# Performance work log

Hardware: AMD Instinct MI355X
Metric: run time of the kernel (lower is better)

Reference implementation:

```python
import jax, jax.numpy as jnp
import numpy as np

B, S, H, L = 8, 4096, 768, 256   # batch, seq_len, hidden_size, num_lines (= line_ids.max()+1)
ATT_HID = 1024                    # attention MLP hidden dim from nn.Linear(hidden,1024)


def setup_inputs() -> dict:
    key = jax.random.key(0)
    k0, k1, k2, k3 = jax.random.split(key, 4)
    token_hidden = jax.random.normal(k0, (B, S, H), dtype=jnp.float32)
    line_ids = jax.random.randint(k1, (B, S), 0, L)  # all valid; -1 would mark invalid
    W1 = jax.random.normal(k2, (H, ATT_HID), dtype=jnp.float32) * 0.02
    b1 = jnp.zeros((ATT_HID,), jnp.float32)
    W2 = jax.random.normal(k3, (ATT_HID, 1), dtype=jnp.float32) * 0.02
    b2 = jnp.zeros((1,), jnp.float32)
    return {"token_hidden": token_hidden, "line_ids": line_ids,
            "W1": W1, "b1": b1, "W2": W2, "b2": b2}


def reference(token_hidden, line_ids, W1, b1, W2, b2):
    b, s, h = token_hidden.shape
    num_lines = L
    n_seg = b * num_lines + 1  # last segment is a dump slot for invalid (-1) tokens

    # attention scores: Linear -> tanh -> Linear, squeeze(-1)  [b, s]
    scores = (jnp.tanh(token_hidden @ W1 + b1) @ W2 + b2)[..., 0]

    valid = (line_ids >= 0).reshape(-1)                                   # [b*s]
    seg = jnp.where(line_ids >= 0,
                    jnp.arange(b)[:, None] * num_lines + line_ids,
                    b * num_lines).reshape(-1)                            # [b*s]
    s_flat = jnp.where(valid, scores.reshape(-1), -jnp.inf)

    # segment-wise stable softmax
    m = jax.ops.segment_max(s_flat, seg, num_segments=n_seg)
    m = jnp.where(jnp.isfinite(m), m, 0.0)  # empty segments -> safe 0
    e = jnp.where(valid, jnp.exp(scores.reshape(-1) - m[seg]), 0.0)
    denom = jax.ops.segment_sum(e, seg, num_segments=n_seg)
    w = e / jnp.maximum(denom[seg], 1e-20)                                # [b*s]

    # weighted sum of tokens per (batch, line) segment
    feats = jax.ops.segment_sum(token_hidden.reshape(-1, h) * w[:, None],
                                seg, num_segments=n_seg)
    line_features = feats[: b * num_lines].reshape(b, num_lines, h)

    counts = jax.ops.segment_sum(valid.astype(jnp.float32), seg, num_segments=n_seg)
    line_mask = counts[: b * num_lines].reshape(b, num_lines) > 0
    return line_features, line_mask
```

## Files before the change

kernel.cpp:

```cpp
#include <hip/hip_runtime.h>
#include <hip/hip_bf16.h>
#include <string.h>

#define M_TOK 32768
#define H_DIM 768
#define AH    1024
#define NSEG  2048
#define LCAP  192
#define CONV_BLOCKS 12288
#define NKT   12

typedef __attribute__((ext_vector_type(8))) __bf16 bf16x8;
typedef __attribute__((ext_vector_type(4))) float f32x4;

__device__ __forceinline__ float tanh_fast(float x) {
  float e = __expf(2.0f * x);
  return 1.0f - 2.0f * __builtin_amdgcn_rcpf(e + 1.0f);
}

__device__ __forceinline__ float bf2f(unsigned short u) {
  unsigned int v = (unsigned int)u << 16;
  float f;
  memcpy(&f, &v, 4);
  return f;
}

__global__ __launch_bounds__(256) void prep_kernel(
    const float* __restrict__ W1, __hip_bfloat16* __restrict__ W1t,
    const float4* __restrict__ X4, uint4* __restrict__ Xb4) {
  __shared__ float tile[32][33];
  if (blockIdx.x < 768) {
    int nt = blockIdx.x & 31, ktile = blockIdx.x >> 5;
    int n0 = nt * 32, k0 = ktile * 32;
    int tx = threadIdx.x & 31, ty = threadIdx.x >> 5;
    for (int r = ty; r < 32; r += 8)
      tile[r][tx] = W1[(size_t)(k0 + r) * AH + n0 + tx];
    __syncthreads();
    for (int r = ty; r < 32; r += 8)
      W1t[(size_t)(n0 + r) * H_DIM + k0 + tx] = __float2bfloat16(tile[tx][r]);
  } else {
    int i = (blockIdx.x - 768) * 256 + threadIdx.x;
    float4 v0 = X4[i * 2];
    float4 v1 = X4[i * 2 + 1];
    __hip_bfloat16 h[8] = {
        __float2bfloat16(v0.x), __float2bfloat16(v0.y),
        __float2bfloat16(v0.z), __float2bfloat16(v0.w),
        __float2bfloat16(v1.x), __float2bfloat16(v1.y),
        __float2bfloat16(v1.z), __float2bfloat16(v1.w)};
    uint4 p;
    memcpy(&p, h, 16);
    Xb4[i] = p;
  }
}

#define WAITV(N) asm volatile("s_waitcnt vmcnt(" #N ")" ::: "memory")
#define WAITL0   asm volatile("s_waitcnt lgkmcnt(0)" ::: "memory")

__global__ __launch_bounds__(512, 2) void attn_score_kernel(
    const __hip_bfloat16* __restrict__ Xbg,
    const __hip_bfloat16* __restrict__ W1tg, const float* __restrict__ b1g,
    const float* __restrict__ W2g, float* __restrict__ scores2) {
  __shared__ __align__(16) __bf16 As[2][256 * 64];
  __shared__ __align__(16) __bf16 Bs[2][256 * 64];

  const int tid = threadIdx.x;
  const int bid = blockIdx.x;
  const int xcd = bid & 7;
  const int sq  = bid >> 3;
  const int m0  = (xcd * 16 + (sq >> 2)) * 256;
  const int ntl = sq & 3;
  const int n0  = ntl * 256;
  const int lane = tid & 63;
  const int wave = tid >> 6;
  const int wm   = wave >> 2;
  const int wx   = wave & 3;
  const int ml   = lane & 15;
  const int lh   = lane >> 4;

  const __bf16* Xb = (const __bf16*)Xbg;
  const __bf16* W  = (const __bf16*)W1tg;

  const int lr   = tid >> 3;
  const int scol = ((tid & 7) ^ (lr & 7)) << 3;

  int aRow[4], bRow[4];
#pragma unroll
  for (int q = 0; q < 4; ++q) {
    aRow[q] = m0 + ((q & 1) << 7) + ((q >> 1) << 6) + lr;
    int lrow = (q << 6) + lr;
    bRow[q] = n0 + (((lrow >> 5) & 3) << 6) + ((lrow >> 7) << 5) + (lrow & 31);
  }

  f32x4 acc[8][4];
#pragma unroll
  for (int i = 0; i < 8; ++i)
#pragma unroll
    for (int j = 0; j < 4; ++j) acc[i][j] = (f32x4)0.f;

#define STAGE_A(q, buf, kt)                                                    \
  __builtin_amdgcn_global_load_lds(                                            \
      (const __attribute__((address_space(1))) void*)(Xb +                     \
          (size_t)aRow[q] * H_DIM + (kt) + scol),                              \
      (__attribute__((address_space(3))) void*)&As[buf][(q) * 4096 + tid * 8], \
      16, 0, 0)
#define STAGE_B(q, buf, kt)                                                    \
  __builtin_amdgcn_global_load_lds(                                            \
      (const __attribute__((address_space(1))) void*)(W +                      \
          (size_t)bRow[q] * H_DIM + (kt) + scol),                              \
      (__attribute__((address_space(3))) void*)&Bs[buf][(q) * 4096 + tid * 8], \
      16, 0, 0)

  STAGE_A(0, 0, 0); STAGE_A(1, 0, 0);
  STAGE_B(0, 0, 0); STAGE_B(1, 0, 0);
  STAGE_A(2, 0, 0); STAGE_A(3, 0, 0);
  STAGE_B(2, 0, 0); STAGE_B(3, 0, 0);

#define PHASE_BODY(Q, P, SS)                                                   \
  {                                                                            \
    __builtin_amdgcn_s_barrier();                                              \
    __builtin_amdgcn_sched_barrier(0);                                         \
    const int mh = (Q) & 1, nh = (Q) >> 1;                                     \
    bf16x8 af[4][2], bfr[2][2];                                                \
    _Pragma("unroll") for (int lf = 0; lf < 4; ++lf) {                         \
      int ra = (mh << 7) + (wm << 6) + (lf << 4) + ml;                         \
      _Pragma("unroll") for (int kk = 0; kk < 2; ++kk) {                       \
        int ph = ((kk << 2) + lh) ^ (ml & 7);                                  \
        af[lf][kk] = *(const bf16x8*)&As[P][(ra << 6) + (ph << 3)];            \
      }                                                                        \
    }                                                                          \
    _Pragma("unroll") for (int jj = 0; jj < 2; ++jj) {                         \
      int rb = (nh << 7) + (wx << 5) + (jj << 4) + ml;                         \
      _Pragma("unroll") for (int kk = 0; kk < 2; ++kk) {                       \
        int ph = ((kk << 2) + lh) ^ (ml & 7);                                  \
        bfr[jj][kk] = *(const bf16x8*)&Bs[P][(rb << 6) + (ph << 3)];           \
      }                                                                        \
    }                                                                          \
    SS;                                                                        \
    WAITL0;                                                                    \
    __builtin_amdgcn_sched_barrier(0);                                         \
    __builtin_amdgcn_s_setprio(1);                                             \
    _Pragma("unroll") for (int lf = 0; lf < 4; ++lf)                           \
      _Pragma("unroll") for (int jj = 0; jj < 2; ++jj)                         \
        _Pragma("unroll") for (int kk = 0; kk < 2; ++kk)                       \
          acc[mh * 4 + lf][nh * 2 + jj] =                                      \
              __builtin_amdgcn_mfma_f32_16x16x32_bf16(                         \
                  af[lf][kk], bfr[jj][kk], acc[mh * 4 + lf][nh * 2 + jj],      \
                  0, 0, 0);                                                    \
    __builtin_amdgcn_s_setprio(0);                                             \
  }

  int p = 0;
  for (int t = 0; t < NKT - 1; ++t) {
    const int ktn = (t + 1) << 6;
    WAITV(4);
    PHASE_BODY(0, p, { STAGE_A(0, p ^ 1, ktn); STAGE_A(1, p ^ 1, ktn); });
    WAITV(4);
    PHASE_BODY(1, p, { STAGE_B(0, p ^ 1, ktn); STAGE_B(1, p ^ 1, ktn); });
    WAITV(4);
    PHASE_BODY(2, p, { STAGE_A(2, p ^ 1, ktn); STAGE_A(3, p ^ 1, ktn); });
    PHASE_BODY(3, p, { STAGE_B(2, p ^ 1, ktn); STAGE_B(3, p ^ 1, ktn); });
    p ^= 1;
  }
  WAITV(4);
  PHASE_BODY(0, p, ((void)0));
  WAITV(2);
  PHASE_BODY(1, p, ((void)0));
  WAITV(0);
  PHASE_BODY(2, p, ((void)0));
  PHASE_BODY(3, p, ((void)0));

  float b1v[4], w2v[4];
#pragma unroll
  for (int nf = 0; nf < 4; ++nf) {
    int n = n0 + wx * 64 + nf * 16 + ml;
    b1v[nf] = b1g[n];
    w2v[nf] = W2g[n];
  }
  float* red = (float*)&As[0][0];
#pragma unroll
  for (int mf = 0; mf < 8; ++mf) {
#pragma unroll
    for (int pp = 0; pp < 4; ++pp) {
      float tsum = 0.f;
#pragma unroll
      for (int nf = 0; nf < 4; ++nf)
        tsum += tanh_fast(acc[mf][nf][pp] + b1v[nf]) * w2v[nf];
      tsum += __shfl_xor(tsum, 1);
      tsum += __shfl_xor(tsum, 2);
      tsum += __shfl_xor(tsum, 4);
      tsum += __shfl_xor(tsum, 8);
      if (ml == 0)
        red[wx * 256 + wm * 128 + mf * 16 + lh * 4 + pp] = tsum;
    }
  }
  __syncthreads();
  if (tid < 256) {
    float v = (red[tid] + red[256 + tid]) + (red[512 + tid] + red[768 + tid]);
    scores2[(size_t)(m0 + tid) * 4 + ntl] = v;
  }
}

__global__ __launch_bounds__(256) void aggregate_kernel(
    const ushort* __restrict__ Xb, const float* __restrict__ scores2,
    const int* __restrict__ line_ids, float4* __restrict__ out4,
    float* __restrict__ out_mask) {
  __shared__ int   slist[LCAP];
  __shared__ float sw[LCAP];
  __shared__ int   wvc[4];
  __shared__ float wred[4];
  const int seg = blockIdx.x;
  const int b = seg >> 8, lid = seg & 255;
  const int tid = threadIdx.x, lane = tid & 63, wave = tid >> 6;
  const int base = b * 4096;

  int ids[16];
#pragma unroll
  for (int c = 0; c < 16; ++c) ids[c] = line_ids[base + c * 256 + tid];

  int total = 0;
#pragma unroll
  for (int c = 0; c < 16; ++c) {
    bool match = (ids[c] == lid);
    unsigned long long mask = __ballot(match);
    if (lane == 0) wvc[wave] = __popcll(mask);
    __syncthreads();
    int off = total;
    for (int w = 0; w < wave; ++w) off += wvc[w];
    if (match) {
      int pos = off + __popcll(mask & ((1ull << lane) - 1ull));
      if (pos < LCAP) slist[pos] = base + c * 256 + tid;
    }
    total += wvc[0] + wvc[1] + wvc[2] + wvc[3];
    __syncthreads();
  }
  int cnt = total > LCAP ? LCAP : total;
  if (tid == 0) out_mask[seg] = cnt > 0 ? 1.f : 0.f;
  if (cnt == 0) {
    if (tid < H_DIM / 4)
      out4[(size_t)seg * (H_DIM / 4) + tid] = make_float4(0.f, 0.f, 0.f, 0.f);
    return;
  }
  float lmax = -3.4e38f;
  if (tid < cnt) {
    const float4 a = *(const float4*)(scores2 + (size_t)slist[tid] * 4);
    float sc = (a.x + a.y) + (a.z + a.w);
    sw[tid] = sc;
    lmax = sc;
  }
#pragma unroll
  for (int d = 1; d < 64; d <<= 1) lmax = fmaxf(lmax, __shfl_xor(lmax, d));
  if (lane == 0) wred[wave] = lmax;
  __syncthreads();
  float m = fmaxf(fmaxf(wred[0], wred[1]), fmaxf(wred[2], wred[3]));
  float lsum = 0.f;
  if (tid < cnt) {
    float e = __expf(sw[tid] - m);
    sw[tid] = e;
    lsum = e;
  }
#pragma unroll
  for (int d = 1; d < 64; d <<= 1) lsum += __shfl_xor(lsum, d);
  __syncthreads();
  if (lane == 0) wred[wave] = lsum;
  __syncthreads();
  float denom = wred[0] + wred[1] + wred[2] + wred[3];
  float inv = __builtin_amdgcn_rcpf(fmaxf(denom, 1e-20f));
  if (tid < cnt) sw[tid] *= inv;
  __syncthreads();
  if (tid < H_DIM / 4) {
    const ushort4* xb = (const ushort4*)Xb + tid;
    float4 acc = make_float4(0.f, 0.f, 0.f, 0.f);
    int t = 0;
    for (; t + 4 <= cnt; t += 4) {
      ushort4 u0 = xb[(size_t)slist[t]     * (H_DIM / 4)];
      ushort4 u1 = xb[(size_t)slist[t + 1] * (H_DIM / 4)];
      ushort4 u2 = xb[(size_t)slist[t + 2] * (H_DIM / 4)];
      ushort4 u3 = xb[(size_t)slist[t + 3] * (H_DIM / 4)];
      float w0 = sw[t], w1 = sw[t + 1], w2 = sw[t + 2], w3 = sw[t + 3];
      acc.x += w0 * bf2f(u0.x) + w1 * bf2f(u1.x) + w2 * bf2f(u2.x) + w3 * bf2f(u3.x);
      acc.y += w0 * bf2f(u0.y) + w1 * bf2f(u1.y) + w2 * bf2f(u2.y) + w3 * bf2f(u3.y);
      acc.z += w0 * bf2f(u0.z) + w1 * bf2f(u1.z) + w2 * bf2f(u2.z) + w3 * bf2f(u3.z);
      acc.w += w0 * bf2f(u0.w) + w1 * bf2f(u1.w) + w2 * bf2f(u2.w) + w3 * bf2f(u3.w);
    }
    for (; t < cnt; ++t) {
      ushort4 u = xb[(size_t)slist[t] * (H_DIM / 4)];
      float w = sw[t];
      acc.x += w * bf2f(u.x); acc.y += w * bf2f(u.y);
      acc.z += w * bf2f(u.z); acc.w += w * bf2f(u.w);
    }
    out4[(size_t)seg * (H_DIM / 4) + tid] = acc;
  }
}

extern "C" void kernel_launch(void* const* d_in, const int* in_sizes, int n_in,
                              void* d_out, int out_size, void* d_ws, size_t ws_size,
                              hipStream_t stream) {
  const float* X        = (const float*)d_in[0];
  const int*   line_ids = (const int*)d_in[1];
  const float* W1       = (const float*)d_in[2];
  const float* b1       = (const float*)d_in[3];
  const float* W2       = (const float*)d_in[4];

  char* p = (char*)d_ws;
  __hip_bfloat16* Xb      = (__hip_bfloat16*)p;  p += (size_t)M_TOK * H_DIM * 2;
  __hip_bfloat16* W1t     = (__hip_bfloat16*)p;  p += 1572864;
  float*          scores2 = (float*)p;           p += (size_t)M_TOK * 4 * 4;

  float* out_feats = (float*)d_out;
  float* out_mask  = out_feats + (size_t)NSEG * H_DIM;

  prep_kernel<<<768 + CONV_BLOCKS, 256, 0, stream>>>(
      W1, W1t, (const float4*)X, (uint4*)Xb);
  attn_score_kernel<<<512, 512, 0, stream>>>(Xb, W1t, b1, W2, scores2);
  aggregate_kernel<<<NSEG, 256, 0, stream>>>((const ushort*)Xb, scores2,
                                             line_ids, (float4*)out_feats,
                                             out_mask);
}
```

Before: 233.0 us.

## Process two N-tiles per block with a continuous pipelined K loop

Each score-GEMM block now covers 512 output columns instead of 256 by running the K loop twice in a single pipeline that flows from the first N half into the second, so the grid is halved to 256 blocks. The main loop is reorganised so fragment reads are reused across quadrants (A or B fragments kept between MFMA groups) and the LDS reads are issued before the barriers. An epilogue runs mid-loop for the first half. The aim is to cut the pipeline prologue and drain overhead per block and the number of LDS fragment reads. The cost is fewer blocks, which may leave CUs underused (256 blocks at 2 per CU), plus extra barriers.

New measurement: 235.7 us. Within noise of the previous version (+1.2%).

```diff
diff --git a/kernel.cpp b/kernel.cpp
--- a/kernel.cpp
+++ b/kernel.cpp
@@ -67,9 +67,8 @@
   const int bid = blockIdx.x;
   const int xcd = bid & 7;
   const int sq  = bid >> 3;
-  const int m0  = (xcd * 16 + (sq >> 2)) * 256;
-  const int ntl = sq & 3;
-  const int n0  = ntl * 256;
+  const int m0  = (xcd * 16 + (sq >> 1)) * 256;
+  const int np0 = (sq & 1) * 512;
   const int lane = tid & 63;
   const int wave = tid >> 6;
   const int wm   = wave >> 2;
@@ -88,7 +87,7 @@
   for (int q = 0; q < 4; ++q) {
     aRow[q] = m0 + ((q & 1) << 7) + ((q >> 1) << 6) + lr;
     int lrow = (q << 6) + lr;
-    bRow[q] = n0 + (((lrow >> 5) & 3) << 6) + ((lrow >> 7) << 5) + (lrow & 31);
+    bRow[q] = np0 + (((lrow >> 5) & 3) << 6) + ((lrow >> 7) << 5) + (lrow & 31);
   }
 
   f32x4 acc[8][4];
@@ -96,6 +95,19 @@
   for (int i = 0; i < 8; ++i)
 #pragma unroll
     for (int j = 0; j < 4; ++j) acc[i][j] = (f32x4)0.f;
+
+  bf16x8 af[4][2], bfr[2][2];
+
+  float b1v[2][4], w2v[2][4];
+#pragma unroll
+  for (int sd = 0; sd < 2; ++sd)
+#pragma unroll
+    for (int nf = 0; nf < 4; ++nf) {
+      int n = np0 + sd * 256 + wx * 64 + nf * 16 + ml;
+      b1v[sd][nf] = b1g[n];
+      w2v[sd][nf] = W2g[n];
+    }
+  WAITV(0);
 
 #define STAGE_A(q, buf, kt)                                                    \
   __builtin_amdgcn_global_load_lds(                                            \
@@ -103,101 +115,153 @@
           (size_t)aRow[q] * H_DIM + (kt) + scol),                              \
       (__attribute__((address_space(3))) void*)&As[buf][(q) * 4096 + tid * 8], \
       16, 0, 0)
-#define STAGE_B(q, buf, kt)                                                    \
+#define STAGE_B(q, buf, kt, nsh)                                               \
   __builtin_amdgcn_global_load_lds(                                            \
       (const __attribute__((address_space(1))) void*)(W +                      \
-          (size_t)bRow[q] * H_DIM + (kt) + scol),                              \
+          (size_t)(bRow[q] + (nsh)) * H_DIM + (kt) + scol),                    \
       (__attribute__((address_space(3))) void*)&Bs[buf][(q) * 4096 + tid * 8], \
       16, 0, 0)
 
-  STAGE_A(0, 0, 0); STAGE_A(1, 0, 0);
-  STAGE_B(0, 0, 0); STAGE_B(1, 0, 0);
-  STAGE_A(2, 0, 0); STAGE_A(3, 0, 0);
-  STAGE_B(2, 0, 0); STAGE_B(3, 0, 0);
-
-#define PHASE_BODY(Q, P, SS)                                                   \
+#define DSRA(MH, P)                                                            \
+  _Pragma("unroll") for (int lf = 0; lf < 4; ++lf) {                           \
+    int ra = ((MH) << 7) + (wm << 6) + (lf << 4) + ml;                         \
+    _Pragma("unroll") for (int kk = 0; kk < 2; ++kk) {                         \
+      int ph = ((kk << 2) + lh) ^ (ml & 7);                                    \
+      af[lf][kk] = *(const bf16x8*)&As[P][(ra << 6) + (ph << 3)];              \
+    }                                                                          \
+  }
+#define DSRB(NH, P)                                                            \
+  _Pragma("unroll") for (int jj = 0; jj < 2; ++jj) {                           \
+    int rb = ((NH) << 7) + (wx << 5) + (jj << 4) + ml;                         \
+    _Pragma("unroll") for (int kk = 0; kk < 2; ++kk) {                         \
+      int ph = ((kk << 2) + lh) ^ (ml & 7);                                    \
+      bfr[jj][kk] = *(const bf16x8*)&Bs[P][(rb << 6) + (ph << 3)];             \
+    }                                                                          \
+  }
+#define MFMAQ(MH, NH)                                                          \
+  __builtin_amdgcn_s_setprio(1);                                               \
+  _Pragma("unroll") for (int kk = 0; kk < 2; ++kk)                             \
+    _Pragma("unroll") for (int lf = 0; lf < 4; ++lf)                           \
+      _Pragma("unroll") for (int jj = 0; jj < 2; ++jj)                         \
+        acc[(MH) * 4 + lf][(NH) * 2 + jj] =                                    \
+            __builtin_amdgcn_mfma_f32_16x16x32_bf16(                           \
+                af[lf][kk], bfr[jj][kk], acc[(MH) * 4 + lf][(NH) * 2 + jj],    \
+                0, 0, 0);                                                      \
+  __builtin_amdgcn_s_setprio(0);
+
+#define BARRIER __builtin_amdgcn_s_barrier()
+#define SCHED0  __builtin_amdgcn_sched_barrier(0)
+
+#define EPILOGUE(side)                                                         \
   {                                                                            \
-    __builtin_amdgcn_s_barrier();                                              \
-    __builtin_amdgcn_sched_barrier(0);                                         \
-    const int mh = (Q) & 1, nh = (Q) >> 1;                                     \
-    bf16x8 af[4][2], bfr[2][2];                                                \
-    _Pragma("unroll") for (int lf = 0; lf < 4; ++lf) {                         \
-      int ra = (mh << 7) + (wm << 6) + (lf << 4) + ml;                         \
-      _Pragma("unroll") for (int kk = 0; kk < 2; ++kk) {                       \
-        int ph = ((kk << 2) + lh) ^ (ml & 7);                                  \
-        af[lf][kk] = *(const bf16x8*)&As[P][(ra << 6) + (ph << 3)];            \
+    __syncthreads();                                                           \
+    float* red = (float*)&As[1][0];                                            \
+    _Pragma("unroll") for (int mf = 0; mf < 8; ++mf) {                         \
+      _Pragma("unroll") for (int pp = 0; pp < 4; ++pp) {                       \
+        float tsum = 0.f;                                                      \
+        _Pragma("unroll") for (int nf = 0; nf < 4; ++nf)                       \
+          tsum += tanh_fast(acc[mf][nf][pp] + b1v[side][nf]) * w2v[side][nf];  \
+        tsum += __shfl_xor(tsum, 1);                                           \
+        tsum += __shfl_xor(tsum, 2);                                           \
+        tsum += __shfl_xor(tsum, 4);                                           \
+        tsum += __shfl_xor(tsum, 8);                                           \
+        if (ml == 0)                                                           \
+          red[wx * 256 + wm * 128 + mf * 16 + lh * 4 + pp] = tsum;             \
       }                                                                        \
     }                                                                          \
-    _Pragma("unroll") for (int jj = 0; jj < 2; ++jj) {                         \
-      int rb = (nh << 7) + (wx << 5) + (jj << 4) + ml;                         \
-      _Pragma("unroll") for (int kk = 0; kk < 2; ++kk) {                       \
-        int ph = ((kk << 2) + lh) ^ (ml & 7);                                  \
-        bfr[jj][kk] = *(const bf16x8*)&Bs[P][(rb << 6) + (ph << 3)];           \
-      }                                                                        \
+    __syncthreads();                                                           \
+    if (tid < 256) {                                                           \
+      float v =                                                                \
+          (red[tid] + red[256 + tid]) + (red[512 + tid] + red[768 + tid]);     \
+      scores2[(size_t)(m0 + tid) * 4 + ((sq & 1) * 2 + (side))] = v;           \
     }                                                                          \
-    SS;                                                                        \
-    WAITL0;                                                                    \
-    __builtin_amdgcn_sched_barrier(0);                                         \
-    __builtin_amdgcn_s_setprio(1);                                             \
-    _Pragma("unroll") for (int lf = 0; lf < 4; ++lf)                           \
-      _Pragma("unroll") for (int jj = 0; jj < 2; ++jj)                         \
-        _Pragma("unroll") for (int kk = 0; kk < 2; ++kk)                       \
-          acc[mh * 4 + lf][nh * 2 + jj] =                                      \
-              __builtin_amdgcn_mfma_f32_16x16x32_bf16(                         \
-                  af[lf][kk], bfr[jj][kk], acc[mh * 4 + lf][nh * 2 + jj],      \
-                  0, 0, 0);                                                    \
-    __builtin_amdgcn_s_setprio(0);                                             \
-  }
-
-  int p = 0;
-  for (int t = 0; t < NKT - 1; ++t) {
-    const int ktn = (t + 1) << 6;
+  }
+
+  STAGE_A(0, 0, 0); STAGE_A(1, 0, 0);
+  STAGE_B(0, 0, 0, 0); STAGE_B(1, 0, 0, 0);
+  STAGE_A(2, 0, 0); STAGE_A(3, 0, 0);
+  STAGE_B(2, 0, 0, 0); STAGE_B(3, 0, 0, 0);
+  WAITV(4);
+  BARRIER;
+
+  int P = 0;
+  for (int tt = 0; tt < 2 * NKT - 1; ++tt) {
+    const int u   = tt + 1;
+    const int ktu = ((u >= NKT) ? (u - NKT) : u) << 6;
+    const int nsh = (u >= NKT) ? 256 : 0;
+
+    DSRA(0, P); DSRB(0, P);
+    STAGE_A(0, P ^ 1, ktu); STAGE_A(1, P ^ 1, ktu);
+    asm volatile("s_waitcnt lgkmcnt(8)" ::: "memory");
+    BARRIER;
+    WAITL0; SCHED0;
+    MFMAQ(0, 0);
     WAITV(4);
-    PHASE_BODY(0, p, { STAGE_A(0, p ^ 1, ktn); STAGE_A(1, p ^ 1, ktn); });
+    BARRIER;
+
+    DSRA(1, P);
+    STAGE_B(0, P ^ 1, ktu, nsh); STAGE_B(1, P ^ 1, ktu, nsh);
+    BARRIER;
+    WAITL0; SCHED0;
+    MFMAQ(1, 0);
     WAITV(4);
-    PHASE_BODY(1, p, { STAGE_B(0, p ^ 1, ktn); STAGE_B(1, p ^ 1, ktn); });
+    BARRIER;
+
+    DSRB(1, P);
+    STAGE_A(2, P ^ 1, ktu); STAGE_A(3, P ^ 1, ktu);
+    BARRIER;
+    WAITL0; SCHED0;
+    MFMAQ(1, 1);
+    BARRIER;
+
+    DSRA(0, P);
+    STAGE_B(2, P ^ 1, ktu, nsh); STAGE_B(3, P ^ 1, ktu, nsh);
+    BARRIER;
+    WAITL0; SCHED0;
+    MFMAQ(0, 1);
     WAITV(4);
-    PHASE_BODY(2, p, { STAGE_A(2, p ^ 1, ktn); STAGE_A(3, p ^ 1, ktn); });
-    PHASE_BODY(3, p, { STAGE_B(2, p ^ 1, ktn); STAGE_B(3, p ^ 1, ktn); });
-    p ^= 1;
-  }
-  WAITV(4);
-  PHASE_BODY(0, p, ((void)0));
+    BARRIER;
+
+    P ^= 1;
+
+    if (tt == NKT - 1) {
+      EPILOGUE(0);
+#pragma unroll
+      for (int i = 0; i < 8; ++i)
+#pragma unroll
+        for (int j = 0; j < 4; ++j) acc[i][j] = (f32x4)0.f;
+      WAITV(0);
+      __syncthreads();
+    }
+  }
+
+  DSRA(0, 1); DSRB(0, 1);
+  asm volatile("s_waitcnt lgkmcnt(8)" ::: "memory");
+  BARRIER;
+  WAITL0; SCHED0;
+  MFMAQ(0, 0);
   WAITV(2);
-  PHASE_BODY(1, p, ((void)0));
+  BARRIER;
+
+  DSRA(1, 1);
+  BARRIER;
+  WAITL0; SCHED0;
+  MFMAQ(1, 0);
   WAITV(0);
-  PHASE_BODY(2, p, ((void)0));
-  PHASE_BODY(3, p, ((void)0));
-
-  float b1v[4], w2v[4];
-#pragma unroll
-  for (int nf = 0; nf < 4; ++nf) {
-    int n = n0 + wx * 64 + nf * 16 + ml;
-    b1v[nf] = b1g[n];
-    w2v[nf] = W2g[n];
-  }
-  float* red = (float*)&As[0][0];
-#pragma unroll
-  for (int mf = 0; mf < 8; ++mf) {
-#pragma unroll
-    for (int pp = 0; pp < 4; ++pp) {
-      float tsum = 0.f;
-#pragma unroll
-      for (int nf = 0; nf < 4; ++nf)
-        tsum += tanh_fast(acc[mf][nf][pp] + b1v[nf]) * w2v[nf];
-      tsum += __shfl_xor(tsum, 1);
-      tsum += __shfl_xor(tsum, 2);
-      tsum += __shfl_xor(tsum, 4);
-      tsum += __shfl_xor(tsum, 8);
-      if (ml == 0)
-        red[wx * 256 + wm * 128 + mf * 16 + lh * 4 + pp] = tsum;
-    }
-  }
-  __syncthreads();
-  if (tid < 256) {
-    float v = (red[tid] + red[256 + tid]) + (red[512 + tid] + red[768 + tid]);
-    scores2[(size_t)(m0 + tid) * 4 + ntl] = v;
-  }
+  BARRIER;
+
+  DSRB(1, 1);
+  BARRIER;
+  WAITL0; SCHED0;
+  MFMAQ(1, 1);
+  BARRIER;
+
+  DSRA(0, 1);
+  BARRIER;
+  WAITL0; SCHED0;
+  MFMAQ(0, 1);
+
+  EPILOGUE(1);
 }
 
 __global__ __launch_bounds__(256) void aggregate_kernel(
@@ -311,7 +375,7 @@
 
   prep_kernel<<<768 + CONV_BLOCKS, 256, 0, stream>>>(
       W1, W1t, (const float4*)X, (uint4*)Xb);
-  attn_score_kernel<<<512, 512, 0, stream>>>(Xb, W1t, b1, W2, scores2);
+  attn_score_kernel<<<256, 512, 0, stream>>>(Xb, W1t, b1, W2, scores2);
   aggregate_kernel<<<NSEG, 256, 0, stream>>>((const ushort*)Xb, scores2,
                                              line_ids, (float4*)out_feats,
                                              out_mask);
```

## Switch score GEMM to 32x32 MFMA with persistent two-pass N tiles per block

Applied to the files above, without the earlier changes.

The attention-score GEMM now uses 32x32x16 bf16 MFMA instead of 16x16x32. Each block covers 512 output columns in two sequential 256-column passes, running the tanh/W2 epilogue between them, so the grid halves to 256 blocks. The four-phase pipeline becomes a single double-buffered loop over 24 k-steps with precomputed pointers and LDS offsets. This aims to cut LDS fragment traffic and launch/tail overhead. In exchange only 256 blocks are launched, which lowers occupancy, and the single WAITV(0) per step may expose load latency.

New measurement: 253.2 us. 1.09x slower.

```diff
diff --git a/kernel.cpp b/kernel.cpp
--- a/kernel.cpp
+++ b/kernel.cpp
@@ -12,6 +12,7 @@
 
 typedef __attribute__((ext_vector_type(8))) __bf16 bf16x8;
 typedef __attribute__((ext_vector_type(4))) float f32x4;
+typedef __attribute__((ext_vector_type(16))) float f32x16;
 
 __device__ __forceinline__ float tanh_fast(float x) {
   float e = __expf(2.0f * x);
@@ -54,7 +55,6 @@
 }
 
 #define WAITV(N) asm volatile("s_waitcnt vmcnt(" #N ")" ::: "memory")
-#define WAITL0   asm volatile("s_waitcnt lgkmcnt(0)" ::: "memory")
 
 __global__ __launch_bounds__(512, 2) void attn_score_kernel(
     const __hip_bfloat16* __restrict__ Xbg,
@@ -67,15 +67,15 @@
   const int bid = blockIdx.x;
   const int xcd = bid & 7;
   const int sq  = bid >> 3;
-  const int m0  = (xcd * 16 + (sq >> 2)) * 256;
-  const int ntl = sq & 3;
-  const int n0  = ntl * 256;
+  const int m0  = (xcd * 16 + (sq >> 1)) * 256;
+  const int np0 = (sq & 1) * 512;
   const int lane = tid & 63;
   const int wave = tid >> 6;
   const int wm   = wave >> 2;
   const int wx   = wave & 3;
-  const int ml   = lane & 15;
-  const int lh   = lane >> 4;
+  const int l31  = lane & 31;
+  const int lk   = lane >> 5;
+  const int l7   = lane & 7;
 
   const __bf16* Xb = (const __bf16*)Xbg;
   const __bf16* W  = (const __bf16*)W1tg;
@@ -83,121 +83,128 @@
   const int lr   = tid >> 3;
   const int scol = ((tid & 7) ^ (lr & 7)) << 3;
 
-  int aRow[4], bRow[4];
+  const __bf16* aP[4];
+  const __bf16* bP[4];
 #pragma unroll
   for (int q = 0; q < 4; ++q) {
-    aRow[q] = m0 + ((q & 1) << 7) + ((q >> 1) << 6) + lr;
-    int lrow = (q << 6) + lr;
-    bRow[q] = n0 + (((lrow >> 5) & 3) << 6) + ((lrow >> 7) << 5) + (lrow & 31);
-  }
-
-  f32x4 acc[8][4];
-#pragma unroll
-  for (int i = 0; i < 8; ++i)
-#pragma unroll
-    for (int j = 0; j < 4; ++j) acc[i][j] = (f32x4)0.f;
-
-#define STAGE_A(q, buf, kt)                                                    \
+    aP[q] = Xb + (size_t)(m0 + (q << 6) + lr) * H_DIM + scol;
+    bP[q] = W + (size_t)(np0 + (q << 6) + lr) * H_DIM + scol;
+  }
+
+  int raBase[4], rbBase[2], physg[4];
+#pragma unroll
+  for (int p = 0; p < 4; ++p) raBase[p] = (wm * 128 + p * 32 + l31) << 6;
+#pragma unroll
+  for (int q = 0; q < 2; ++q) rbBase[q] = (wx * 64 + q * 32 + l31) << 6;
+#pragma unroll
+  for (int ks = 0; ks < 4; ++ks) physg[ks] = (((ks << 1) + lk) ^ l7) << 3;
+
+  f32x16 acc[4][2];
+#pragma unroll
+  for (int p = 0; p < 4; ++p)
+#pragma unroll
+    for (int q = 0; q < 2; ++q) acc[p][q] = (f32x16)0.f;
+
+  float b1v[2][2], w2v[2][2];
+#pragma unroll
+  for (int sd = 0; sd < 2; ++sd)
+#pragma unroll
+    for (int q = 0; q < 2; ++q) {
+      int n = np0 + sd * 256 + wx * 64 + q * 32 + l31;
+      b1v[sd][q] = b1g[n];
+      w2v[sd][q] = W2g[n];
+    }
+  WAITV(0);
+
+#define STAGE_A(q, buf, off)                                                   \
   __builtin_amdgcn_global_load_lds(                                            \
-      (const __attribute__((address_space(1))) void*)(Xb +                     \
-          (size_t)aRow[q] * H_DIM + (kt) + scol),                              \
+      (const __attribute__((address_space(1))) void*)(aP[q] + (off)),          \
       (__attribute__((address_space(3))) void*)&As[buf][(q) * 4096 + tid * 8], \
       16, 0, 0)
-#define STAGE_B(q, buf, kt)                                                    \
+#define STAGE_B(q, buf, off)                                                   \
   __builtin_amdgcn_global_load_lds(                                            \
-      (const __attribute__((address_space(1))) void*)(W +                      \
-          (size_t)bRow[q] * H_DIM + (kt) + scol),                              \
+      (const __attribute__((address_space(1))) void*)(bP[q] + (off)),          \
       (__attribute__((address_space(3))) void*)&Bs[buf][(q) * 4096 + tid * 8], \
       16, 0, 0)
 
-  STAGE_A(0, 0, 0); STAGE_A(1, 0, 0);
-  STAGE_B(0, 0, 0); STAGE_B(1, 0, 0);
-  STAGE_A(2, 0, 0); STAGE_A(3, 0, 0);
-  STAGE_B(2, 0, 0); STAGE_B(3, 0, 0);
-
-#define PHASE_BODY(Q, P, SS)                                                   \
+#define EPILOGUE(side)                                                         \
   {                                                                            \
-    __builtin_amdgcn_s_barrier();                                              \
-    __builtin_amdgcn_sched_barrier(0);                                         \
-    const int mh = (Q) & 1, nh = (Q) >> 1;                                     \
-    bf16x8 af[4][2], bfr[2][2];                                                \
-    _Pragma("unroll") for (int lf = 0; lf < 4; ++lf) {                         \
-      int ra = (mh << 7) + (wm << 6) + (lf << 4) + ml;                         \
-      _Pragma("unroll") for (int kk = 0; kk < 2; ++kk) {                       \
-        int ph = ((kk << 2) + lh) ^ (ml & 7);                                  \
-        af[lf][kk] = *(const bf16x8*)&As[P][(ra << 6) + (ph << 3)];            \
+    __syncthreads();                                                           \
+    float* red = (float*)&As[1][0];                                            \
+    _Pragma("unroll") for (int p = 0; p < 4; ++p) {                            \
+      _Pragma("unroll") for (int rg = 0; rg < 16; ++rg) {                      \
+        float v = tanh_fast(acc[p][0][rg] + b1v[side][0]) * w2v[side][0] +     \
+                  tanh_fast(acc[p][1][rg] + b1v[side][1]) * w2v[side][1];      \
+        v += __shfl_xor(v, 1);                                                 \
+        v += __shfl_xor(v, 2);                                                 \
+        v += __shfl_xor(v, 4);                                                 \
+        v += __shfl_xor(v, 8);                                                 \
+        v += __shfl_xor(v, 16);                                                \
+        if (l31 == 0) {                                                        \
+          int row = wm * 128 + p * 32 + (rg & 3) + ((rg >> 2) << 3) + (lk << 2); \
+          red[wx * 256 + row] = v;                                             \
+        }                                                                      \
       }                                                                        \
     }                                                                          \
-    _Pragma("unroll") for (int jj = 0; jj < 2; ++jj) {                         \
-      int rb = (nh << 7) + (wx << 5) + (jj << 4) + ml;                         \
-      _Pragma("unroll") for (int kk = 0; kk < 2; ++kk) {                       \
-        int ph = ((kk << 2) + lh) ^ (ml & 7);                                  \
-        bfr[jj][kk] = *(const bf16x8*)&Bs[P][(rb << 6) + (ph << 3)];           \
-      }                                                                        \
+    __syncthreads();                                                           \
+    if (tid < 256) {                                                           \
+      float v =                                                                \
+          (red[tid] + red[256 + tid]) + (red[512 + tid] + red[768 + tid]);     \
+      scores2[(size_t)(m0 + tid) * 4 + ((sq & 1) * 2 + (side))] = v;           \
     }                                                                          \
-    SS;                                                                        \
-    WAITL0;                                                                    \
-    __builtin_amdgcn_sched_barrier(0);                                         \
-    __builtin_amdgcn_s_setprio(1);                                             \
-    _Pragma("unroll") for (int lf = 0; lf < 4; ++lf)                           \
-      _Pragma("unroll") for (int jj = 0; jj < 2; ++jj)                         \
-        _Pragma("unroll") for (int kk = 0; kk < 2; ++kk)                       \
-          acc[mh * 4 + lf][nh * 2 + jj] =                                      \
-              __builtin_amdgcn_mfma_f32_16x16x32_bf16(                         \
-                  af[lf][kk], bfr[jj][kk], acc[mh * 4 + lf][nh * 2 + jj],      \
-                  0, 0, 0);                                                    \
-    __builtin_amdgcn_s_setprio(0);                                             \
-  }
-
-  int p = 0;
-  for (int t = 0; t < NKT - 1; ++t) {
-    const int ktn = (t + 1) << 6;
-    WAITV(4);
-    PHASE_BODY(0, p, { STAGE_A(0, p ^ 1, ktn); STAGE_A(1, p ^ 1, ktn); });
-    WAITV(4);
-    PHASE_BODY(1, p, { STAGE_B(0, p ^ 1, ktn); STAGE_B(1, p ^ 1, ktn); });
-    WAITV(4);
-    PHASE_BODY(2, p, { STAGE_A(2, p ^ 1, ktn); STAGE_A(3, p ^ 1, ktn); });
-    PHASE_BODY(3, p, { STAGE_B(2, p ^ 1, ktn); STAGE_B(3, p ^ 1, ktn); });
-    p ^= 1;
-  }
-  WAITV(4);
-  PHASE_BODY(0, p, ((void)0));
-  WAITV(2);
-  PHASE_BODY(1, p, ((void)0));
+    __syncthreads();                                                           \
+  }
+
+  STAGE_A(0, 0, 0); STAGE_A(1, 0, 0); STAGE_A(2, 0, 0); STAGE_A(3, 0, 0);
+  STAGE_B(0, 0, 0); STAGE_B(1, 0, 0); STAGE_B(2, 0, 0); STAGE_B(3, 0, 0);
   WAITV(0);
-  PHASE_BODY(2, p, ((void)0));
-  PHASE_BODY(3, p, ((void)0));
-
-  float b1v[4], w2v[4];
-#pragma unroll
-  for (int nf = 0; nf < 4; ++nf) {
-    int n = n0 + wx * 64 + nf * 16 + ml;
-    b1v[nf] = b1g[n];
-    w2v[nf] = W2g[n];
-  }
-  float* red = (float*)&As[0][0];
-#pragma unroll
-  for (int mf = 0; mf < 8; ++mf) {
-#pragma unroll
-    for (int pp = 0; pp < 4; ++pp) {
-      float tsum = 0.f;
-#pragma unroll
-      for (int nf = 0; nf < 4; ++nf)
-        tsum += tanh_fast(acc[mf][nf][pp] + b1v[nf]) * w2v[nf];
-      tsum += __shfl_xor(tsum, 1);
-      tsum += __shfl_xor(tsum, 2);
-      tsum += __shfl_xor(tsum, 4);
-      tsum += __shfl_xor(tsum, 8);
-      if (ml == 0)
-        red[wx * 256 + wm * 128 + mf * 16 + lh * 4 + pp] = tsum;
-    }
-  }
-  __syncthreads();
-  if (tid < 256) {
-    float v = (red[tid] + red[256 + tid]) + (red[512 + tid] + red[768 + tid]);
-    scores2[(size_t)(m0 + tid) * 4 + ntl] = v;
-  }
+  __builtin_amdgcn_s_barrier();
+  __builtin_amdgcn_sched_barrier(0);
+
+#pragma unroll 2
+  for (int tt = 0; tt < 2 * NKT; ++tt) {
+    const int P = tt & 1;
+    if (tt < 2 * NKT - 1) {
+      const int u = tt + 1;
+      const int ktu = ((u >= NKT) ? (u - NKT) : u) << 6;
+      const int boff = ((u >= NKT) ? 256 * H_DIM : 0) + ktu;
+      STAGE_A(0, P ^ 1, ktu); STAGE_A(1, P ^ 1, ktu);
+      STAGE_A(2, P ^ 1, ktu); STAGE_A(3, P ^ 1, ktu);
+      STAGE_B(0, P ^ 1, boff); STAGE_B(1, P ^ 1, boff);
+      STAGE_B(2, P ^ 1, boff); STAGE_B(3, P ^ 1, boff);
+    }
+#pragma unroll
+    for (int ks = 0; ks < 4; ++ks) {
+      bf16x8 a0 = *(const bf16x8*)&As[P][raBase[0] + physg[ks]];
+      bf16x8 a1 = *(const bf16x8*)&As[P][raBase[1] + physg[ks]];
+      bf16x8 a2 = *(const bf16x8*)&As[P][raBase[2] + physg[ks]];
+      bf16x8 a3 = *(const bf16x8*)&As[P][raBase[3] + physg[ks]];
+      bf16x8 b0 = *(const bf16x8*)&Bs[P][rbBase[0] + physg[ks]];
+      bf16x8 b1f = *(const bf16x8*)&Bs[P][rbBase[1] + physg[ks]];
+      __builtin_amdgcn_s_setprio(1);
+      acc[0][0] = __builtin_amdgcn_mfma_f32_32x32x16_bf16(a0, b0, acc[0][0], 0, 0, 0);
+      acc[1][0] = __builtin_amdgcn_mfma_f32_32x32x16_bf16(a1, b0, acc[1][0], 0, 0, 0);
+      acc[2][0] = __builtin_amdgcn_mfma_f32_32x32x16_bf16(a2, b0, acc[2][0], 0, 0, 0);
+      acc[3][0] = __builtin_amdgcn_mfma_f32_32x32x16_bf16(a3, b0, acc[3][0], 0, 0, 0);
+      acc[0][1] = __builtin_amdgcn_mfma_f32_32x32x16_bf16(a0, b1f, acc[0][1], 0, 0, 0);
+      acc[1][1] = __builtin_amdgcn_mfma_f32_32x32x16_bf16(a1, b1f, acc[1][1], 0, 0, 0);
+      acc[2][1] = __builtin_amdgcn_mfma_f32_32x32x16_bf16(a2, b1f, acc[2][1], 0, 0, 0);
+      acc[3][1] = __builtin_amdgcn_mfma_f32_32x32x16_bf16(a3, b1f, acc[3][1], 0, 0, 0);
+      __builtin_amdgcn_s_setprio(0);
+    }
+    WAITV(0);
+    __builtin_amdgcn_s_barrier();
+    __builtin_amdgcn_sched_barrier(0);
+    if (tt == NKT - 1) {
+      EPILOGUE(0);
+#pragma unroll
+      for (int p = 0; p < 4; ++p)
+#pragma unroll
+        for (int q = 0; q < 2; ++q) acc[p][q] = (f32x16)0.f;
+    }
+  }
+
+  EPILOGUE(1);
 }
 
 __global__ __launch_bounds__(256) void aggregate_kernel(
@@ -311,7 +318,7 @@
 
   prep_kernel<<<768 + CONV_BLOCKS, 256, 0, stream>>>(
       W1, W1t, (const float4*)X, (uint4*)Xb);
-  attn_score_kernel<<<512, 512, 0, stream>>>(Xb, W1t, b1, W2, scores2);
+  attn_score_kernel<<<256, 512, 0, stream>>>(Xb, W1t, b1, W2, scores2);
   aggregate_kernel<<<NSEG, 256, 0, stream>>>((const ushort*)Xb, scores2,
                                              line_ids, (float4*)out_feats,
                                              out_mask);
```
